# Kernel optimization log

Hardware: AMD Instinct MI355X
Metric: run time of the kernel (lower is better)

The kernel has to match this reference:

```python
import jax, jax.numpy as jnp
import numpy as np

IMG_H, IMG_W = 512.0, 512.0
PRE_NMS = 2000   # training-mode pre_nms_top_n
POST_NMS = 2000  # training-mode post_nms_top_n
NMS_THRESH = 0.7
SCORE_THRESH = 0.0
MIN_SIZE = 0.001


def setup_inputs() -> dict:
    key = jax.random.key(0)
    k1, k2, k3 = jax.random.split(key, 3)
    N = 8
    num_anchors_per_level = (49152, 12288, 3072, 768, 192)  # strides 4..64, 3 anchors/loc on 512^2
    A = sum(num_anchors_per_level)
    cxy = jax.random.uniform(k1, (N, A, 2), minval=0.0, maxval=512.0)
    wh = jax.random.uniform(k2, (N, A, 2), minval=2.0, maxval=120.0)
    proposals = jnp.concatenate([cxy - wh / 2, cxy + wh / 2], axis=-1)  # xyxy
    objectness = jax.random.normal(k3, (N, A), dtype=jnp.float32)
    return {"proposals": proposals, "objectness": objectness,
            "num_anchors_per_level": num_anchors_per_level}


def _box_iou(a, b):
    # a: [K,4], b: [K,4] -> [K,K] pairwise IoU (torchvision box_iou semantics)
    area_a = (a[:, 2] - a[:, 0]) * (a[:, 3] - a[:, 1])
    area_b = (b[:, 2] - b[:, 0]) * (b[:, 3] - b[:, 1])
    lt = jnp.maximum(a[:, None, :2], b[None, :, :2])
    rb = jnp.minimum(a[:, None, 2:], b[None, :, 2:])
    wh = jnp.clip(rb - lt, 0.0)
    inter = wh[..., 0] * wh[..., 1]
    return inter / (area_a[:, None] + area_b[None, :] - inter)


def _per_image(boxes, scores, lvl):
    # boxes [K,4] xyxy, scores [K] (sigmoid probs), lvl [K] int32 level ids
    # 1) clip to image
    x = jnp.clip(boxes[:, 0::2], 0.0, IMG_W)
    y = jnp.clip(boxes[:, 1::2], 0.0, IMG_H)
    boxes = jnp.stack([x[:, 0], y[:, 0], x[:, 1], y[:, 1]], axis=-1)
    # 2) small-box + 3) score-threshold masks (masking instead of boolean indexing)
    ws = boxes[:, 2] - boxes[:, 0]
    hs = boxes[:, 3] - boxes[:, 1]
    valid = (ws >= MIN_SIZE) & (hs >= MIN_SIZE) & (scores >= SCORE_THRESH)
    # 4) batched NMS: offset boxes per level so levels never overlap
    off = lvl.astype(boxes.dtype) * (jnp.max(boxes) + 1.0)
    off_boxes = boxes + off[:, None]
    sm = jnp.where(valid, scores, -jnp.inf)
    order = jnp.argsort(-sm)                 # descending score, invalid last
    boxes_s = boxes[order]
    scores_s = scores[order]
    valid_s = valid[order]
    ob_s = jax.lax.stop_gradient(off_boxes[order])
    K = ob_s.shape[0]
    iou = _box_iou(ob_s, ob_s)               # [K,K], keep decision is non-differentiable
    j = jnp.arange(K)
    def body(i, keep):
        suppress = keep[i] & (iou[i] > NMS_THRESH) & (j > i)
        return keep & ~suppress
    keep = jax.lax.fori_loop(0, K, body, valid_s)
    # 5) top post_nms kept boxes, padded to fixed size with zeros
    rank = jnp.cumsum(keep.astype(jnp.int32)) - 1
    sel_key = jnp.where(keep & (rank < POST_NMS), rank, K)
    idx = jnp.argsort(sel_key)[:POST_NMS]
    out_valid = sel_key[idx] < K
    out_boxes = jnp.where(out_valid[:, None], boxes_s[idx], 0.0)
    out_scores = jnp.where(out_valid, scores_s[idx], 0.0)
    return out_boxes, out_scores


def _forward(proposals, objectness, num_anchors_per_level):
    N = proposals.shape[0]
    napl = [int(n) for n in num_anchors_per_level]
    # per-level, per-image top-k on objectness (get_top_n_idx)
    idx_list, lv_list, off = [], [], 0
    for i, n in enumerate(napl):
        k = min(PRE_NMS, n)
        _, ti = jax.lax.top_k(objectness[:, off:off + n], k)
        idx_list.append(ti + off)
        lv_list.append(jnp.full((k,), i, dtype=jnp.int32))
        off += n
    top_idx = jnp.concatenate(idx_list, axis=1)   # [N, K_total]
    lvls = jnp.concatenate(lv_list)               # [K_total], same for every image
    bidx = jnp.arange(N)[:, None]
    obj = objectness[bidx, top_idx]
    props = proposals[bidx, top_idx]
    scores = jax.nn.sigmoid(obj)
    return jax.vmap(lambda b, s: _per_image(b, s, lvls))(props, scores)


def reference(proposals, objectness, num_anchors_per_level):
    # returns (boxes [N, POST_NMS, 4], scores [N, POST_NMS]); invalid slots zero-padded
    return _forward(proposals, objectness, num_anchors_per_level)
```

## Files before the change

kernel.cpp:

```cpp
#include <hip/hip_runtime.h>
#include <math.h>

#define NIMG 8
#define ATOT 65472
#define KTOT 6960
#define POST 2000
#define TILES_PER_IMG 1668
#define NTILES (NIMG*TILES_PER_IMG)
#define ESEG 1024
#define M_TIE 0.7000000178813934326171875
#define PAD(i) ((i) + ((i) >> 5))

__constant__ int c_NAPL[5]  = {49152,12288,3072,768,192};
__constant__ int c_LOFF[5]  = {0,49152,61440,64512,65280};
__constant__ int c_KSEL[5]  = {2000,2000,2000,768,192};
__constant__ int c_CBASE[5] = {0,2000,4000,6000,6768};
__constant__ int c_GLVL[5]  = {32,32,32,12,3};
__constant__ int c_TILEPFX[6] = {0,528,1056,1584,1662,1668};

__device__ __forceinline__ unsigned f2u(float f){
  unsigned b = __float_as_uint(f);
  return (b & 0x80000000u) ? ~b : (b | 0x80000000u);
}
__device__ __forceinline__ unsigned long long mkkey(unsigned u, unsigned gidx){
  return ((unsigned long long)u << 32) | (unsigned long long)(0xFFFFFFFFu - gidx);
}

extern "C" __global__ void __launch_bounds__(1024)
k_select(const float* __restrict__ prop, const float* __restrict__ obj,
         unsigned long long* __restrict__ cand, float4* __restrict__ cbox,
         unsigned* __restrict__ zzone){
  __shared__ unsigned long long sb[2112];
  __shared__ unsigned hist[4096];
  __shared__ unsigned csum[256];
  __shared__ unsigned h8[256];
  __shared__ unsigned s_b12, s_cumAbove, s_t20, s_cnt;
  int task = blockIdx.x, img = task/5, lvl = task%5;
  int n = c_NAPL[lvl], k = c_KSEL[lvl], tid = threadIdx.x;
  if (task == 0)
    for (int i = tid; i < 1280; i += 1024) zzone[i] = 0u;

  const float4* o4 = (const float4*)(obj + (size_t)img*ATOT + c_LOFF[lvl]);
  int n4 = n >> 2;
  unsigned T = 0u;
  if (k < n){
    for (int i = tid; i < 4096; i += 1024) hist[i] = 0u;
    if (tid < 256) h8[tid] = 0u;
    __syncthreads();
    for (int i = tid; i < n4; i += 1024){
      float4 v = o4[i];
      atomicAdd(&hist[f2u(v.x) >> 20], 1u);
      atomicAdd(&hist[f2u(v.y) >> 20], 1u);
      atomicAdd(&hist[f2u(v.z) >> 20], 1u);
      atomicAdd(&hist[f2u(v.w) >> 20], 1u);
    }
    __syncthreads();
    if (tid < 256){
      unsigned s = 0;
      for (int j = 0; j < 16; ++j) s += hist[tid*16 + j];
      csum[tid] = s;
    }
    __syncthreads();
    if (tid == 0){
      unsigned kk = (unsigned)k, cum = 0, b12 = 0;
      for (int c = 255; c >= 0; --c){
        if (cum + csum[c] >= kk){
          for (int j = 15; j >= 0; --j){
            unsigned bv = hist[c*16 + j];
            if (cum + bv >= kk){ b12 = (unsigned)(c*16 + j); break; }
            cum += bv;
          }
          break;
        }
        cum += csum[c];
      }
      s_b12 = b12; s_cumAbove = cum;
    }
    __syncthreads();
    unsigned b12 = s_b12;
    for (int i = tid; i < n4; i += 1024){
      float4 v = o4[i];
      unsigned ux = f2u(v.x), uy = f2u(v.y), uz = f2u(v.z), uw = f2u(v.w);
      if ((ux >> 20) == b12) atomicAdd(&h8[(ux >> 12) & 255u], 1u);
      if ((uy >> 20) == b12) atomicAdd(&h8[(uy >> 12) & 255u], 1u);
      if ((uz >> 20) == b12) atomicAdd(&h8[(uz >> 12) & 255u], 1u);
      if ((uw >> 20) == b12) atomicAdd(&h8[(uw >> 12) & 255u], 1u);
    }
    __syncthreads();
    if (tid == 0){
      unsigned kk = (unsigned)k, cum = s_cumAbove, t20 = (s_b12 << 8);
      for (int j = 255; j >= 0; --j){
        cum += h8[j];
        if (cum >= kk){ t20 = (s_b12 << 8) | (unsigned)j; break; }
      }
      s_t20 = t20;
    }
    __syncthreads();
    T = s_t20;
  }
  if (tid == 0) s_cnt = 0u;
  __syncthreads();
  int abase = c_LOFF[lvl];
  for (int i = tid; i < n4; i += 1024){
    float4 v = o4[i];
    float vv[4] = {v.x, v.y, v.z, v.w};
    #pragma unroll
    for (int c2 = 0; c2 < 4; ++c2){
      unsigned u = f2u(vv[c2]);
      if ((u >> 12) >= T){
        unsigned p = atomicAdd(&s_cnt, 1u);
        if (p < 2048u) sb[PAD(p)] = mkkey(u, (unsigned)(abase + i*4 + c2));
      }
    }
  }
  __syncthreads();
  int cnt = (int)min(s_cnt, 2048u);
  int m = 256; while (m < k || m < cnt) m <<= 1;
  for (int i = cnt + tid; i < m; i += 1024) sb[PAD(i)] = 0ull;
  __syncthreads();
  for (int size = 2; size <= m; size <<= 1){
    for (int stride = size >> 1; stride > 0; stride >>= 1){
      for (int t = tid; t < (m >> 1); t += 1024){
        int lo = t & (stride - 1);
        int i  = ((t - lo) << 1) + lo;
        int j  = i + stride;
        bool desc = ((i & size) == 0);
        unsigned long long a = sb[PAD(i)], b = sb[PAD(j)];
        if (desc ? (a < b) : (a > b)){ sb[PAD(i)] = b; sb[PAD(j)] = a; }
      }
      __syncthreads();
    }
  }
  const float4* pr = (const float4*)(prop + (size_t)img*ATOT*4);
  for (int i = tid; i < k; i += 1024){
    unsigned long long key = sb[PAD(i)];
    size_t slot = (size_t)img*KTOT + c_CBASE[lvl] + i;
    cand[slot] = key;
    unsigned gidx = 0xFFFFFFFFu - (unsigned)(key & 0xFFFFFFFFull);
    float4 p = pr[gidx];
    cbox[slot] = make_float4(fminf(fmaxf(p.x,0.f),512.f), fminf(fmaxf(p.y,0.f),512.f),
                             fminf(fmaxf(p.z,0.f),512.f), fminf(fmaxf(p.w,0.f),512.f));
  }
}

extern "C" __global__ void __launch_bounds__(64)
k_mask(const float4* __restrict__ cbox, unsigned* __restrict__ ecnt,
       unsigned* __restrict__ eseg, float4* __restrict__ out4, int out_n4){
  __shared__ float4 colb[64];
  __shared__ float  colA[64];
  int bid = blockIdx.x, lane = threadIdx.x;
  if (bid < 313){
    int i = bid*64 + lane;
    if (i < out_n4) out4[i] = make_float4(0.f,0.f,0.f,0.f);
  }
  int img = bid / TILES_PER_IMG, r = bid % TILES_PER_IMG;
  int lvl = 0;
  while (r >= c_TILEPFX[lvl + 1]) ++lvl;
  int t = r - c_TILEPFX[lvl];
  int G = c_GLVL[lvl], k = c_KSEL[lvl];
  int gi = 0;
  while (t >= G - gi){ t -= G - gi; ++gi; }
  int gj = gi + t;
  int task = img*5 + lvl;
  const float4* cb = cbox + (size_t)img*KTOT + c_CBASE[lvl];

  int jj = gj*64 + lane;
  float4 bb = (jj < k) ? cb[jj] : make_float4(0.f,0.f,0.f,0.f);
  colb[lane] = bb;
  colA[lane] = (bb.z - bb.x) * (bb.w - bb.y);
  __syncthreads();

  int i = gi*64 + lane;
  unsigned long long word = 0ull;
  if (i < k){
    float4 a = cb[i];
    float aarea = (a.z - a.x) * (a.w - a.y);
    for (int j = 0; j < 64; ++j){
      float4 b = colb[j];
      float ix = fminf(a.z, b.z) - fmaxf(a.x, b.x);
      float iy = fminf(a.w, b.w) - fmaxf(a.y, b.y);
      float inter = ix * iy;
      float uni = (aarea + colA[j]) - inter;
      bool hit = (ix > 0.f) & (iy > 0.f) & ((double)inter >= M_TIE * (double)uni);
      word |= hit ? (1ull << j) : 0ull;
    }
    if (gi == gj)
      word &= (lane == 63) ? 0ull : (~0ull << (lane + 1));
  }
  int nb = __popcll(word);
  int pfx = nb;
  for (int d = 1; d < 64; d <<= 1){
    int v = __shfl_up(pfx, d);
    if (lane >= d) pfx += v;
  }
  int total = __shfl(pfx, 63);
  if (total > 0){
    unsigned base = 0;
    if (lane == 0) base = atomicAdd(&ecnt[task*32 + gi], (unsigned)total);
    base = __shfl(base, 0);
    unsigned idx = base + (unsigned)(pfx - nb);
    unsigned* ep = eseg + (size_t)(task*32 + gi)*ESEG;
    while (word){
      int j = __ffsll(word) - 1; word &= word - 1;
      if (idx < ESEG) ep[idx] = ((unsigned)i << 16) | (unsigned)(gj*64 + j);
      ++idx;
    }
  }
}

extern "C" __global__ void __launch_bounds__(64)
k_scan(const unsigned long long* __restrict__ cand, const unsigned* __restrict__ ecnt,
       const unsigned* __restrict__ eseg, unsigned long long* __restrict__ clist,
       unsigned* __restrict__ ccnt){
  __shared__ unsigned ledge[6144];
  __shared__ unsigned soff[33], wpfx[33];
  __shared__ unsigned long long sm[64];
  __shared__ unsigned long long remW[32], keepW[32];
  __shared__ unsigned long long s_hasI;
  int task = blockIdx.x, img = task / 5, lvl = task % 5;
  int k = c_KSEL[lvl], nW = c_GLVL[lvl], tid = threadIdx.x;

  if (tid == 0){
    unsigned s = 0;
    for (int w = 0; w < nW; ++w){ soff[w] = s; s += min(ecnt[task*32 + w], (unsigned)ESEG); }
    soff[nW] = s;
  }
  if (tid < 32) remW[tid] = 0ull;
  __syncthreads();
  for (int w = 0; w < nW; ++w){
    unsigned c = soff[w+1] - soff[w];
    const unsigned* ep = eseg + (size_t)(task*32 + w)*ESEG;
    for (unsigned e = tid; e < c; e += 64){
      unsigned p = soff[w] + e;
      if (p < 6144u) ledge[p] = ep[e];
    }
  }
  __syncthreads();

  for (int w = 0; w < nW; ++w){
    unsigned c = soff[w+1] - soff[w];
    if (c == 0) continue;
    const unsigned* ep = eseg + (size_t)(task*32 + w)*ESEG;
    sm[tid] = 0ull;
    if (tid == 0) s_hasI = 0ull;
    __syncthreads();
    for (unsigned e = tid; e < c; e += 64){
      unsigned p = soff[w] + e;
      unsigned ed = (p < 6144u) ? ledge[p] : ep[e];
      int i = (int)(ed >> 16), j = (int)(ed & 0xFFFFu);
      if ((j >> 6) == w){
        atomicOr(&sm[i & 63], 1ull << (j & 63));
        atomicOr(&s_hasI, 1ull << (i & 63));
      }
    }
    __syncthreads();
    if (tid == 0){
      unsigned long long r = remW[w];
      unsigned long long x = s_hasI & ~r;
      while (x){
        int i = __ffsll(x) - 1;
        r |= sm[i];
        x &= ~(1ull << i);
        x &= ~r;
      }
      remW[w] = r;
    }
    __syncthreads();
    unsigned long long keep_w = ~remW[w];
    for (unsigned e = tid; e < c; e += 64){
      unsigned p = soff[w] + e;
      unsigned ed = (p < 6144u) ? ledge[p] : ep[e];
      int i = (int)(ed >> 16), j = (int)(ed & 0xFFFFu), wj = j >> 6;
      if (wj != w && ((keep_w >> (i & 63)) & 1ull))
        atomicOr(&remW[wj], 1ull << (j & 63));
    }
    __syncthreads();
  }

  if (tid < 32){
    unsigned long long v = 0ull;
    if (tid < nW){
      int rem = k - tid*64;
      v = (rem >= 64) ? ~0ull : ((1ull << rem) - 1ull);
    }
    keepW[tid] = v & ~remW[tid];
  }
  __syncthreads();
  if (tid == 0){
    unsigned s = 0;
    for (int w = 0; w < nW; ++w){ wpfx[w] = s; s += (unsigned)__popcll(keepW[w]); }
    ccnt[task] = s;
  }
  __syncthreads();
  size_t base = (size_t)img*KTOT + c_CBASE[lvl];
  for (int i = tid; i < k; i += 64){
    unsigned long long w = keepW[i >> 6];
    if ((w >> (i & 63)) & 1ull){
      unsigned long long lowmask = (i & 63) ? ((1ull << (i & 63)) - 1ull) : 0ull;
      unsigned rank = wpfx[i >> 6] + (unsigned)__popcll(w & lowmask);
      clist[base + rank] = cand[base + i];
    }
  }
}

__device__ __forceinline__ int cntGreater(const unsigned long long* base, int len,
                                          unsigned long long x){
  int lo = 0, hi = len;
  while (lo < hi){
    int mid = (lo + hi) >> 1;
    if (base[mid] > x) lo = mid + 1; else hi = mid;
  }
  return lo;
}

extern "C" __global__ void __launch_bounds__(1024)
k_merge(const float* __restrict__ prop, const float* __restrict__ obj,
        const unsigned long long* __restrict__ clist, const unsigned* __restrict__ ccnt,
        float* __restrict__ out){
  __shared__ unsigned long long keys[KTOT];
  __shared__ int loff[6], lcnt[5];
  int img = blockIdx.x >> 3, eighth = blockIdx.x & 7, tid = threadIdx.x;
  if (tid == 0){
    int s = 0;
    for (int l = 0; l < 5; ++l){ lcnt[l] = (int)ccnt[img*5 + l]; loff[l] = s; s += lcnt[l]; }
    loff[5] = s;
  }
  __syncthreads();
  for (int l = 0; l < 5; ++l){
    size_t gb = (size_t)img*KTOT + c_CBASE[l];
    int c = lcnt[l], lo = loff[l];
    for (int e = tid; e < c; e += 1024) keys[lo + e] = clist[gb + e];
  }
  __syncthreads();
  const float4* pr = (const float4*)(prop + (size_t)img*ATOT*4);
  const float*  o  = obj + (size_t)img*ATOT;
  float* ob = out + (size_t)img*POST*4;
  float* os = out + (size_t)NIMG*POST*4 + (size_t)img*POST;
  int tot = loff[5];
  for (int tt = tid; ; tt += 1024){
    int t = 8*tt + eighth;
    if (t >= tot) break;
    int lvl = 0;
    while (t >= loff[lvl + 1]) ++lvl;
    unsigned long long x = keys[t];
    int pos = t - loff[lvl];
    for (int l = 0; l < 5; ++l){
      if (l == lvl) continue;
      pos += cntGreater(keys + loff[l], lcnt[l], x);
    }
    if (pos < POST){
      unsigned gidx = 0xFFFFFFFFu - (unsigned)(x & 0xFFFFFFFFull);
      float4 p = pr[gidx];
      ob[pos*4 + 0] = fminf(fmaxf(p.x, 0.f), 512.f);
      ob[pos*4 + 1] = fminf(fmaxf(p.y, 0.f), 512.f);
      ob[pos*4 + 2] = fminf(fmaxf(p.z, 0.f), 512.f);
      ob[pos*4 + 3] = fminf(fmaxf(p.w, 0.f), 512.f);
      double sgm = 1.0 / (1.0 + exp(-(double)o[gidx]));
      os[pos] = (float)sgm;
    }
  }
}

extern "C" void kernel_launch(void* const* d_in, const int* in_sizes, int n_in,
                              void* d_out, int out_size, void* d_ws, size_t ws_size,
                              hipStream_t stream){
  const float* prop = (const float*)d_in[0];
  const float* obj  = (const float*)d_in[1];
  char* ws = (char*)d_ws;
  unsigned*           ecnt = (unsigned*)(ws);
  unsigned*           ccnt = (unsigned*)(ws + 5120);
  unsigned long long* cand = (unsigned long long*)(ws + 5632);
  unsigned long long* clist= (unsigned long long*)(ws + 451072);
  float4*             cbox = (float4*)(ws + 896512);
  unsigned*           eseg = (unsigned*)(ws + 1787392);

  int out_n4 = out_size / 4;
  hipLaunchKernelGGL(k_select, dim3(40),  dim3(1024), 0, stream, prop, obj, cand, cbox, ecnt);
  hipLaunchKernelGGL(k_mask,   dim3(NTILES), dim3(64), 0, stream, cbox, ecnt, eseg,
                     (float4*)d_out, out_n4);
  hipLaunchKernelGGL(k_scan,   dim3(40),  dim3(64),   0, stream, cand, ecnt, eseg, clist, ccnt);
  hipLaunchKernelGGL(k_merge,  dim3(64),  dim3(1024), 0, stream, prop, obj, clist, ccnt, (float*)d_out);
}
```

Before: 200.3 us.

## Parallelize radix threshold scans, aggregate compaction atomics, and add float fast-path IoU test

The serial single-thread bucket searches in the top-k selection are replaced with block-wide parallel suffix scans over the 12-bit and 8-bit histograms. Candidate compaction now uses a wavefront ballot with one atomic per wave instead of one shared-memory atomic per element. In the IoU bitmask kernel, a float comparison with a small margin decides most pairs, and the exact double-precision tie test runs only when some lane in the wave is near the threshold. The scans add many barriers, and the band test adds a wave vote in the inner loop.

New measurement: 202.2 us. Within noise of the previous version (+0.9%).

```diff
diff --git a/kernel.cpp b/kernel.cpp
--- a/kernel.cpp
+++ b/kernel.cpp
@@ -32,7 +32,7 @@
          unsigned* __restrict__ zzone){
   __shared__ unsigned long long sb[2112];
   __shared__ unsigned hist[4096];
-  __shared__ unsigned csum[256];
+  __shared__ unsigned scan[1024];
   __shared__ unsigned h8[256];
   __shared__ unsigned s_b12, s_cumAbove, s_t20, s_cnt;
   int task = blockIdx.x, img = task/5, lvl = task%5;
@@ -42,6 +42,7 @@
 
   const float4* o4 = (const float4*)(obj + (size_t)img*ATOT + c_LOFF[lvl]);
   int n4 = n >> 2;
+  unsigned kk = (unsigned)k;
   unsigned T = 0u;
   if (k < n){
     for (int i = tid; i < 4096; i += 1024) hist[i] = 0u;
@@ -55,26 +56,27 @@
       atomicAdd(&hist[f2u(v.w) >> 20], 1u);
     }
     __syncthreads();
-    if (tid < 256){
-      unsigned s = 0;
-      for (int j = 0; j < 16; ++j) s += hist[tid*16 + j];
-      csum[tid] = s;
-    }
-    __syncthreads();
-    if (tid == 0){
-      unsigned kk = (unsigned)k, cum = 0, b12 = 0;
-      for (int c = 255; c >= 0; --c){
-        if (cum + csum[c] >= kk){
-          for (int j = 15; j >= 0; --j){
-            unsigned bv = hist[c*16 + j];
-            if (cum + bv >= kk){ b12 = (unsigned)(c*16 + j); break; }
-            cum += bv;
-          }
-          break;
-        }
-        cum += csum[c];
+    unsigned own[4]; unsigned s = 0;
+    int b0 = tid*4;
+    #pragma unroll
+    for (int j = 0; j < 4; ++j){ own[j] = hist[b0+j]; s += own[j]; }
+    scan[tid] = s;
+    __syncthreads();
+    for (int d = 1; d < 1024; d <<= 1){
+      unsigned v = (tid + d < 1024) ? scan[tid + d] : 0u;
+      __syncthreads();
+      scan[tid] += v;
+      __syncthreads();
+    }
+    {
+      unsigned R = scan[tid] - s;
+      unsigned sufn = R;
+      #pragma unroll
+      for (int j = 3; j >= 0; --j){
+        unsigned sufj = sufn + own[j];
+        if (sufj >= kk && sufn < kk){ s_b12 = (unsigned)(b0 + j); s_cumAbove = sufn; }
+        sufn = sufj;
       }
-      s_b12 = b12; s_cumAbove = cum;
     }
     __syncthreads();
     unsigned b12 = s_b12;
@@ -87,13 +89,19 @@
       if ((uw >> 20) == b12) atomicAdd(&h8[(uw >> 12) & 255u], 1u);
     }
     __syncthreads();
-    if (tid == 0){
-      unsigned kk = (unsigned)k, cum = s_cumAbove, t20 = (s_b12 << 8);
-      for (int j = 255; j >= 0; --j){
-        cum += h8[j];
-        if (cum >= kk){ t20 = (s_b12 << 8) | (unsigned)j; break; }
-      }
-      s_t20 = t20;
+    if (tid < 256) scan[tid] = h8[tid];
+    __syncthreads();
+    for (int d = 1; d < 256; d <<= 1){
+      unsigned v = 0;
+      if (tid < 256) v = (tid + d < 256) ? scan[tid + d] : 0u;
+      __syncthreads();
+      if (tid < 256) scan[tid] += v;
+      __syncthreads();
+    }
+    if (tid < 256){
+      unsigned sufj = s_cumAbove + scan[tid];
+      unsigned sufn = s_cumAbove + ((tid < 255) ? scan[tid + 1] : 0u);
+      if (sufj >= kk && sufn < kk) s_t20 = (s_b12 << 8) | (unsigned)tid;
     }
     __syncthreads();
     T = s_t20;
@@ -101,14 +109,21 @@
   if (tid == 0) s_cnt = 0u;
   __syncthreads();
   int abase = c_LOFF[lvl];
+  int lane = tid & 63;
   for (int i = tid; i < n4; i += 1024){
     float4 v = o4[i];
     float vv[4] = {v.x, v.y, v.z, v.w};
     #pragma unroll
     for (int c2 = 0; c2 < 4; ++c2){
       unsigned u = f2u(vv[c2]);
-      if ((u >> 12) >= T){
-        unsigned p = atomicAdd(&s_cnt, 1u);
+      bool pred = (u >> 12) >= T;
+      unsigned long long bm = __ballot(pred);
+      unsigned cw = (unsigned)__popcll(bm);
+      unsigned basep = 0;
+      if (lane == 0 && cw) basep = atomicAdd(&s_cnt, cw);
+      basep = __shfl(basep, 0);
+      if (pred){
+        unsigned p = basep + (unsigned)__popcll(bm & ((1ull << lane) - 1ull));
         if (p < 2048u) sb[PAD(p)] = mkkey(u, (unsigned)(abase + i*4 + c2));
       }
     }
@@ -181,7 +196,13 @@
       float iy = fminf(a.w, b.w) - fmaxf(a.y, b.y);
       float inter = ix * iy;
       float uni = (aarea + colA[j]) - inter;
-      bool hit = (ix > 0.f) & (iy > 0.f) & ((double)inter >= M_TIE * (double)uni);
+      bool base = (ix > 0.f) & (iy > 0.f);
+      bool hi  = inter >= 0.701f * uni;
+      bool lo  = inter <  0.699f * uni;
+      bool hit = base & hi;
+      bool amb = base & (!hi) & (!lo);
+      if (__any(amb))
+        hit = hit | (amb & ((double)inter >= M_TIE * (double)uni));
       word |= hit ? (1ull << j) : 0ull;
     }
     if (gi == gj)
```
